# Optimization experiments

Hardware: AMD Instinct MI355X
Metric: run time of the kernel (lower is better)

## Reference

```python
import jax, jax.numpy as jnp
import numpy as np

VERY_NEG = -1e30
N_HEADS = 8


def _dag_attention(leaves, ancestors, mask, w1, b1, w2, b2):
    # leaves/ancestors: [C, A, H], mask: [C, A]
    m = mask[..., None]                                   # [C, A, 1]
    x = jnp.concatenate([leaves * m, ancestors * m], -1)  # [C, A, 2H]
    x = jax.nn.relu(x @ w1 + b1)                          # [C, A, H]
    s = x @ w2 + b2 + (1.0 - m) * VERY_NEG                # [C, A, 1]
    a = jax.nn.softmax(s, axis=1)
    return (a * ancestors * m).sum(axis=1)                # [C, H]


def _encoder_layer(x, mask4d, wq, wk, wv, wo, fw1, fb1, fw2, fb2):
    B, S, H = x.shape
    d = H // N_HEADS
    q = (x @ wq).reshape(B, S, N_HEADS, d)
    k = (x @ wk).reshape(B, S, N_HEADS, d)
    v = (x @ wv).reshape(B, S, N_HEADS, d)
    scores = jnp.einsum('bqhd,bkhd->bhqk', q, k) / jnp.sqrt(jnp.float32(d)) + mask4d
    attn = jax.nn.softmax(scores, axis=-1)
    ctx = jnp.einsum('bhqk,bkhd->bqhd', attn, v).reshape(B, S, H)
    x = x + ctx @ wo
    x = x + jax.nn.relu(x @ fw1 + fb1) @ fw2 + fb2
    return x


def _attention_pooling(x, mask3d, pw, pb):
    # x: [B, S, H], mask3d: [B, S, 1] additive mask
    s = x @ pw + pb + mask3d           # [B, S, 1]
    a = jax.nn.softmax(s, axis=1)
    return (a * x).sum(axis=1)          # [B, H]


def setup_inputs() -> dict:
    key = jax.random.key(0)
    ks = jax.random.split(key, 32)
    B, S, H, C, NODES, A = 128, 256, 256, 20000, 25000, 8

    def w(k, shape, scale=0.02):
        return (jax.random.normal(k, shape, jnp.float32) * scale)

    input_ids = jax.random.randint(ks[0], (B, S), 0, C)
    code_mask = (jax.random.uniform(ks[1], (B, S)) < 0.9).astype(jnp.float32)
    code_mask = code_mask.at[:, 0].set(1.0)
    dx_leaves_list = jax.random.randint(ks[2], (C, A), 0, NODES)
    dx_ancestors_list = jax.random.randint(ks[3], (C, A), 0, NODES)
    dx_masks_list = (jax.random.uniform(ks[4], (C, A)) < 0.8).astype(jnp.float32)
    dx_masks_list = dx_masks_list.at[:, 0].set(1.0)

    inp = dict(
        input_ids=input_ids, code_mask=code_mask,
        dx_leaves_list=dx_leaves_list, dx_ancestors_list=dx_ancestors_list,
        dx_masks_list=dx_masks_list,
        embed_init_w=w(ks[5], (NODES + 1, H)).at[NODES].set(0.0),  # padding row
        embed_inputs_w=w(ks[6], (C + 1, H)).at[C].set(0.0),
        attn_w1=w(ks[7], (2 * H, H)), attn_b1=jnp.zeros((H,), jnp.float32),
        attn_w2=w(ks[8], (H, 1)), attn_b2=jnp.zeros((1,), jnp.float32),
        pool_w=w(ks[9], (H, 1)), pool_b=jnp.zeros((1,), jnp.float32),
    )
    names = ['visit', 'dag']
    for i, nm in enumerate(names):
        base = 10 + 6 * i
        inp[nm + '_wq'] = w(ks[base], (H, H))
        inp[nm + '_wk'] = w(ks[base + 1], (H, H))
        inp[nm + '_wv'] = w(ks[base + 2], (H, H))
        inp[nm + '_wo'] = w(ks[base + 3], (H, H))
        inp[nm + '_fw1'] = w(ks[base + 4], (H, 4 * H))
        inp[nm + '_fb1'] = jnp.zeros((4 * H,), jnp.float32)
        inp[nm + '_fw2'] = w(ks[base + 5], (4 * H, H))
        inp[nm + '_fb2'] = jnp.zeros((H,), jnp.float32)
    return inp


def reference(input_ids, code_mask, dx_leaves_list, dx_ancestors_list, dx_masks_list,
              embed_init_w, embed_inputs_w, attn_w1, attn_b1, attn_w2, attn_b2,
              pool_w, pool_b,
              visit_wq, visit_wk, visit_wv, visit_wo, visit_fw1, visit_fb1, visit_fw2, visit_fb2,
              dag_wq, dag_wk, dag_wv, dag_wo, dag_fw1, dag_fb1, dag_fw2, dag_fb2):
    H = embed_init_w.shape[1]
    # Full-vocabulary DAG embedding recomputation (gather -> MLP -> masked softmax -> weighted sum)
    leaves_emb = embed_init_w[dx_leaves_list]          # [C, A, H]
    ancestors_emb = embed_init_w[dx_ancestors_list]    # [C, A, H]
    dag_emb = _dag_attention(leaves_emb, ancestors_emb, dx_masks_list,
                             attn_w1, attn_b1, attn_w2, attn_b2)   # [C, H]
    dict_matrix = jnp.concatenate([jnp.zeros((1, H), jnp.float32), dag_emb], axis=0)

    inputs = embed_inputs_w[input_ids]       # [B, S, H]
    inputs_dag = dict_matrix[input_ids]      # [B, S, H]

    ext_mask = (1.0 - code_mask)[:, None, None, :] * VERY_NEG  # [B,1,1,S]
    visit_outs = _encoder_layer(inputs, ext_mask, visit_wq, visit_wk, visit_wv, visit_wo,
                                visit_fw1, visit_fb1, visit_fw2, visit_fb2)
    dag_hidden = _encoder_layer(inputs_dag, ext_mask, dag_wq, dag_wk, dag_wv, dag_wo,
                                dag_fw1, dag_fb1, dag_fw2, dag_fb2)

    pool_mask = (1.0 - code_mask)[:, :, None] * VERY_NEG       # [B,S,1]
    dag_outs = _attention_pooling(dag_hidden, pool_mask, pool_w, pool_b)
    return (visit_outs, dag_outs)
```

## Files before the change

kernel.cpp:

```cpp
#include <hip/hip_runtime.h>
#include <hip/hip_bf16.h>
#include <math.h>

#define VERY_NEG (-1e30f)

constexpr int Bc = 128, Sc = 256, Hc = 256, Cc = 20000, Ac = 8, NHc = 8, DHc = 32, FFc = 1024;
constexpr int Mc = Bc * Sc;
constexpr int Rc = Cc * Ac;

typedef __attribute__((ext_vector_type(8))) short short8;
typedef __attribute__((ext_vector_type(4))) float floatx4;

static __device__ __forceinline__ unsigned short f2bf(float f) {
  union { float f; unsigned u; } v; v.f = f;
  unsigned r = v.u + 0x7FFF + ((v.u >> 16) & 1);
  return (unsigned short)(r >> 16);
}
static __device__ __forceinline__ unsigned pack2(float lo, float hi) {
  return (unsigned)f2bf(lo) | ((unsigned)f2bf(hi) << 16);
}
static __device__ __forceinline__ float bf2f(unsigned short u) {
  union { unsigned u; float f; } v; v.u = ((unsigned)u) << 16; return v.f;
}

static __device__ __forceinline__ void glds16(const unsigned short* g,
                                              unsigned short* l) {
  __builtin_amdgcn_global_load_lds(
      (const __attribute__((address_space(1))) void*)g,
      (__attribute__((address_space(3))) void*)l, 16, 0, 0);
}

__global__ __launch_bounds__(256) void prep_weights(
    const float* __restrict__ wq, const float* __restrict__ wk,
    const float* __restrict__ wv, const float* __restrict__ wo,
    const float* __restrict__ fw1, const float* __restrict__ fw2,
    unsigned short* __restrict__ qkvT, unsigned short* __restrict__ woT,
    unsigned short* __restrict__ fw1T, unsigned short* __restrict__ fw2T) {
  int gid = blockIdx.x * 256 + threadIdx.x;
  if (gid < 196608) {
    int which = gid >> 16, rem = gid & 65535;
    int n = rem >> 8, k = rem & 255;
    const float* w = which == 0 ? wq : (which == 1 ? wk : wv);
    qkvT[gid] = f2bf(w[k * 256 + n]);
  } else if (gid < 262144) {
    int rem = gid - 196608;
    int n = rem >> 8, k = rem & 255;
    woT[rem] = f2bf(wo[k * 256 + n]);
  } else if (gid < 524288) {
    int rem = gid - 262144;
    int n = rem >> 8, k = rem & 255;
    fw1T[rem] = f2bf(fw1[k * 1024 + n]);
  } else {
    int rem = gid - 524288;
    int n = rem >> 10, k = rem & 1023;
    fw2T[rem] = f2bf(fw2[k * 256 + n]);
  }
}

template <int K, bool BIAS, bool RELU, bool RESID, int OUT>
__global__ __launch_bounds__(256) void gemm_mfma(
    const unsigned short* __restrict__ A, const unsigned short* __restrict__ Bt,
    const float* __restrict__ bias, const float* __restrict__ resid,
    float* __restrict__ Cf, unsigned short* __restrict__ C2, int N) {
  __shared__ unsigned short As[128 * 64];
  __shared__ unsigned short Bs[128 * 64];
  const int tid = threadIdx.x;
  const int nwg = gridDim.x * gridDim.y;
  const int bid0 = blockIdx.y * gridDim.x + blockIdx.x;
  const int swz = (bid0 & 7) * (nwg >> 3) + (bid0 >> 3);
  const int rowBase = (swz / gridDim.x) * 128;
  const int colBase = (swz % gridDim.x) * 128;
  const int wave = tid >> 6, lane = tid & 63;
  const int wm = wave >> 1, wn = wave & 1;
  const int quad = lane >> 4, l15 = lane & 15;
  const int s8 = (((lane & 7) ^ (lane >> 3)) << 3);
  const int rs0 = (wave << 5) + (lane >> 3);
  const int swzf = l15 & 7;

  floatx4 acc[4][4];
#pragma unroll
  for (int mt = 0; mt < 4; ++mt)
#pragma unroll
    for (int nt = 0; nt < 4; ++nt) acc[mt][nt] = (floatx4){0.f, 0.f, 0.f, 0.f};

  for (int k0 = 0; k0 < K; k0 += 64) {
#pragma unroll
    for (int i = 0; i < 4; ++i) {
      int r = rs0 + (i << 3);
      int lb = wave * 2048 + i * 512;
      glds16(A + (size_t)(rowBase + r) * K + k0 + s8, &As[lb]);
      glds16(Bt + (size_t)(colBase + r) * K + k0 + s8, &Bs[lb]);
    }
    __syncthreads();
#pragma unroll
    for (int kk = 0; kk < 2; ++kk) {
      short8 af[4], bfr[4];
#pragma unroll
      for (int mt = 0; mt < 4; ++mt)
        af[mt] = *(const short8*)&As[(wm * 64 + mt * 16 + l15) * 64 +
                                     ((((kk << 2) | quad) ^ swzf) << 3)];
#pragma unroll
      for (int nt = 0; nt < 4; ++nt)
        bfr[nt] = *(const short8*)&Bs[(wn * 64 + nt * 16 + l15) * 64 +
                                      ((((kk << 2) | quad) ^ swzf) << 3)];
#pragma unroll
      for (int mt = 0; mt < 4; ++mt)
#pragma unroll
        for (int nt = 0; nt < 4; ++nt)
          acc[mt][nt] = __builtin_amdgcn_mfma_f32_16x16x32_bf16(
              af[mt], bfr[nt], acc[mt][nt], 0, 0, 0);
    }
    __syncthreads();
  }

#pragma unroll
  for (int mt = 0; mt < 4; ++mt) {
#pragma unroll
    for (int nt = 0; nt < 4; ++nt) {
      int col = colBase + wn * 64 + nt * 16 + l15;
      float bz = BIAS ? bias[col] : 0.f;
#pragma unroll
      for (int i = 0; i < 4; ++i) {
        int row = rowBase + wm * 64 + mt * 16 + quad * 4 + i;
        float v = acc[mt][nt][i];
        if (BIAS) v += bz;
        if (RELU) v = fmaxf(v, 0.f);
        if (RESID) v += resid[(size_t)row * N + col];
        if (OUT == 0) {
          Cf[(size_t)row * N + col] = v;
        } else if (OUT == 1) {
          C2[(size_t)row * N + col] = f2bf(v);
        } else if (OUT == 2) {
          Cf[(size_t)row * N + col] = v;
          C2[(size_t)row * N + col] = f2bf(v);
        } else {
          C2[(size_t)(col >> 8) * 16777216 + (size_t)row * 256 + (col & 255)] =
              f2bf(v);
        }
      }
    }
  }
}

__global__ __launch_bounds__(256, 2) void ffn_fused(
    const unsigned short* __restrict__ A, const unsigned short* __restrict__ w1T,
    const unsigned short* __restrict__ w2T, const float* __restrict__ b1,
    const float* __restrict__ b2, const float* __restrict__ resid,
    float* __restrict__ outC) {
  __shared__ unsigned short Xs[4][4096];
  __shared__ unsigned short Ws[16384];
  __shared__ unsigned short Hs[2][4096];
  const int tid = threadIdx.x;
  const int wave = tid >> 6, lane = tid & 63;
  const int wm = wave >> 1, wn = wave & 1;
  const int quad = lane >> 4, l15 = lane & 15;
  const int s8 = (((lane & 7) ^ (lane >> 3)) << 3);
  const int rs0x = (wave << 4) + (lane >> 3);
  const int rs0 = (wave << 5) + (lane >> 3);
  const int rs0b = (wave << 6) + (lane >> 3);
  const int swzf = l15 & 7;
  const int rowBase = blockIdx.x * 64;

#pragma unroll
  for (int kc = 0; kc < 4; ++kc)
#pragma unroll
    for (int i = 0; i < 2; ++i) {
      int r = rs0x + (i << 3);
      glds16(A + (size_t)(rowBase + r) * 256 + kc * 64 + s8,
             &Xs[kc][wave * 1024 + i * 512]);
    }

  floatx4 acc2[2][8];
#pragma unroll
  for (int mt = 0; mt < 2; ++mt)
#pragma unroll
    for (int nt = 0; nt < 8; ++nt) acc2[mt][nt] = (floatx4){0.f, 0.f, 0.f, 0.f};

  for (int nb = 0; nb < 8; ++nb) {
    floatx4 hacc[2][4];
#pragma unroll
    for (int mt = 0; mt < 2; ++mt)
#pragma unroll
      for (int nt = 0; nt < 4; ++nt) hacc[mt][nt] = (floatx4){0.f, 0.f, 0.f, 0.f};

#pragma unroll
    for (int hf = 0; hf < 2; ++hf) {
#pragma unroll
      for (int kc = 0; kc < 2; ++kc)
#pragma unroll
        for (int i = 0; i < 4; ++i) {
          int r = rs0 + (i << 3);
          glds16(w1T + (size_t)(nb * 128 + r) * 256 + (hf * 2 + kc) * 64 + s8,
                 &Ws[kc * 8192 + wave * 2048 + i * 512]);
        }
      __syncthreads();
#pragma unroll
      for (int kc = 0; kc < 2; ++kc) {
        int kg = hf * 2 + kc;
#pragma unroll
        for (int kk = 0; kk < 2; ++kk) {
          short8 af[2], bfr[4];
#pragma unroll
          for (int mt = 0; mt < 2; ++mt)
            af[mt] = *(const short8*)&Xs[kg][(wm * 32 + mt * 16 + l15) * 64 +
                                            ((((kk << 2) | quad) ^ swzf) << 3)];
#pragma unroll
          for (int nt = 0; nt < 4; ++nt)
            bfr[nt] = *(const short8*)&Ws[kc * 8192 +
                                          (wn * 64 + nt * 16 + l15) * 64 +
                                          ((((kk << 2) | quad) ^ swzf) << 3)];
#pragma unroll
          for (int mt = 0; mt < 2; ++mt)
#pragma unroll
            for (int nt = 0; nt < 4; ++nt)
              hacc[mt][nt] = __builtin_amdgcn_mfma_f32_16x16x32_bf16(
                  af[mt], bfr[nt], hacc[mt][nt], 0, 0, 0);
        }
      }
      __syncthreads();
    }

    float b1v[4];
#pragma unroll
    for (int nt = 0; nt < 4; ++nt)
      b1v[nt] = b1[nb * 128 + wn * 64 + nt * 16 + l15];
#pragma unroll
    for (int mt = 0; mt < 2; ++mt)
#pragma unroll
      for (int nt = 0; nt < 4; ++nt) {
        int nh = wn * 64 + nt * 16 + l15;
        int kc2 = nh >> 6, c6 = nh & 63;
#pragma unroll
        for (int i = 0; i < 4; ++i) {
          int row = wm * 32 + mt * 16 + quad * 4 + i;
          float hv = fmaxf(hacc[mt][nt][i] + b1v[nt], 0.f);
          Hs[kc2][row * 64 + ((((c6 >> 3) ^ (row & 7)) << 3) | (c6 & 7))] =
              f2bf(hv);
        }
      }
#pragma unroll
    for (int i = 0; i < 8; ++i) {
      int r = rs0b + (i << 3);
      glds16(w2T + (size_t)r * 1024 + nb * 128 + s8,
             &Ws[wave * 4096 + i * 512]);
    }
    __syncthreads();

#pragma unroll
    for (int kc2 = 0; kc2 < 2; ++kc2) {
      if (kc2 == 1) {
        __syncthreads();
#pragma unroll
        for (int i = 0; i < 8; ++i) {
          int r = rs0b + (i << 3);
          glds16(w2T + (size_t)r * 1024 + nb * 128 + 64 + s8,
                 &Ws[wave * 4096 + i * 512]);
        }
        __syncthreads();
      }
#pragma unroll
      for (int kk = 0; kk < 2; ++kk) {
        short8 pf[2], bfr2[8];
#pragma unroll
        for (int mt = 0; mt < 2; ++mt)
          pf[mt] = *(const short8*)&Hs[kc2][(wm * 32 + mt * 16 + l15) * 64 +
                                            ((((kk << 2) | quad) ^ swzf) << 3)];
#pragma unroll
        for (int nt = 0; nt < 8; ++nt)
          bfr2[nt] = *(const short8*)&Ws[(wn * 128 + nt * 16 + l15) * 64 +
                                         ((((kk << 2) | quad) ^ swzf) << 3)];
#pragma unroll
        for (int mt = 0; mt < 2; ++mt)
#pragma unroll
          for (int nt = 0; nt < 8; ++nt)
            acc2[mt][nt] = __builtin_amdgcn_mfma_f32_16x16x32_bf16(
                pf[mt], bfr2[nt], acc2[mt][nt], 0, 0, 0);
      }
    }
    __syncthreads();
  }

#pragma unroll
  for (int mt = 0; mt < 2; ++mt)
#pragma unroll
    for (int nt = 0; nt < 8; ++nt) {
      int col = wn * 128 + nt * 16 + l15;
      float bz = b2[col];
#pragma unroll
      for (int i = 0; i < 4; ++i) {
        int row = rowBase + wm * 32 + mt * 16 + quad * 4 + i;
        outC[(size_t)row * 256 + col] =
            acc2[mt][nt][i] + bz + resid[(size_t)row * 256 + col];
      }
    }
}

__global__ __launch_bounds__(256) void cvt_emb16(
    const float* __restrict__ emb, unsigned short* __restrict__ e16) {
  int gid = blockIdx.x * 256 + threadIdx.x;
  int base = gid * 8;
  int row = base >> 8;
  uint4 o;
  if (row < 25001) {
    float4 a = *(const float4*)(emb + base);
    float4 b = *(const float4*)(emb + base + 4);
    o.x = pack2(a.x, a.y); o.y = pack2(a.z, a.w);
    o.z = pack2(b.x, b.y); o.w = pack2(b.z, b.w);
  } else {
    o = (uint4){0u, 0u, 0u, 0u};
  }
  *(uint4*)(e16 + base) = o;
}

__global__ __launch_bounds__(256) void prep_w1T_pq(
    const float* __restrict__ w1, unsigned short* __restrict__ Bt) {
  int gid = blockIdx.x * 256 + threadIdx.x;
  int n = gid >> 8, k = gid & 255;
  float v = (n < 256) ? w1[k * 256 + n] : w1[(256 + k) * 256 + (n - 256)];
  Bt[gid] = f2bf(v);
}

__global__ __launch_bounds__(256) void dag_score(
    const int* __restrict__ leaves, const int* __restrict__ anc,
    const unsigned short* __restrict__ PQ, const float* __restrict__ b1,
    const float* __restrict__ w2, float* __restrict__ s) {
  const int tid = threadIdx.x;
  const int l16 = tid & 15;
  const int r = blockIdx.x * 16 + (tid >> 4);

  float b1c[16], w2c[16];
#pragma unroll
  for (int j = 0; j < 4; ++j) {
    *(float4*)&b1c[j * 4] = *(const float4*)(b1 + l16 * 16 + j * 4);
    *(float4*)&w2c[j * 4] = *(const float4*)(w2 + l16 * 16 + j * 4);
  }

  const int nl = leaves[r], na = anc[r];
  const unsigned short* pp = PQ + (size_t)nl * 512 + l16 * 16;
  const unsigned short* qp = PQ + (size_t)na * 512 + 256 + l16 * 16;

  float acc = 0.f;
#pragma unroll
  for (int half = 0; half < 2; ++half) {
    uint4 pv = *(const uint4*)(pp + half * 8);
    uint4 qv = *(const uint4*)(qp + half * 8);
    const unsigned short* pu = (const unsigned short*)&pv;
    const unsigned short* qu = (const unsigned short*)&qv;
#pragma unroll
    for (int j = 0; j < 8; ++j) {
      float h = bf2f(pu[j]) + bf2f(qu[j]) + b1c[half * 8 + j];
      acc += fmaxf(h, 0.f) * w2c[half * 8 + j];
    }
  }
  acc += __shfl_xor(acc, 1, 64);
  acc += __shfl_xor(acc, 2, 64);
  acc += __shfl_xor(acc, 4, 64);
  acc += __shfl_xor(acc, 8, 64);
  if (l16 == 0) s[r] = acc;
}

__global__ __launch_bounds__(256) void dag_finalize(
    const float* __restrict__ s, const float* __restrict__ masks,
    const int* __restrict__ anc, const float* __restrict__ b2,
    const unsigned short* __restrict__ emb16, float* __restrict__ dict) {
  const int c = blockIdx.x;
  const int t = threadIdx.x;
  __shared__ float sv[8], mv[8];
  __shared__ int nv[8];
  if (t < 8) {
    int idx = c * 8 + t;
    float m = masks[idx];
    sv[t] = s[idx] + b2[0] + (1.f - m) * VERY_NEG;
    mv[t] = m;
    nv[t] = anc[idx];
  }
  __syncthreads();
  float mx = -INFINITY;
#pragma unroll
  for (int a = 0; a < 8; ++a) mx = fmaxf(mx, sv[a]);
  float e[8], sum = 0.f;
#pragma unroll
  for (int a = 0; a < 8; ++a) { e[a] = __expf(sv[a] - mx); sum += e[a]; }
  float inv = 1.f / sum;
  float o = 0.f;
#pragma unroll
  for (int a = 0; a < 8; ++a)
    o += e[a] * inv * mv[a] * bf2f(emb16[(size_t)nv[a] * 256 + t]);
  dict[(size_t)(c + 1) * 256 + t] = o;
  if (c == 0) dict[t] = 0.f;
}

__global__ __launch_bounds__(256) void gather_both(
    const int* __restrict__ ids, const float4* __restrict__ table,
    float4* __restrict__ outf, unsigned short* __restrict__ outb) {
  int gid = blockIdx.x * 256 + threadIdx.x;
  int row = gid >> 6;
  int c4 = gid & 63;
  float4 v = table[(size_t)ids[row] * 64 + c4];
  outf[gid] = v;
  uint2 o;
  o.x = pack2(v.x, v.y);
  o.y = pack2(v.z, v.w);
  *(uint2*)(outb + (size_t)gid * 4) = o;
}

static __device__ __forceinline__ int vt_addr(int d, int col) {
  return d * 272 + ((((col) * 2) ^ (((d >> 3) & 3) << 4)) >> 1);
}
static __device__ __forceinline__ int ps_addr(int row, int col) {
  return row * 40 + ((((col) * 2) ^ (((row >> 2) & 3) << 4)) >> 1);
}

__global__ __launch_bounds__(256, 4) void attn_mfma(
    const unsigned short* __restrict__ q, const unsigned short* __restrict__ k,
    const unsigned short* __restrict__ v, const float* __restrict__ cm,
    unsigned short* __restrict__ ctx) {
  __shared__ unsigned short Vt[32 * 272];
  __shared__ unsigned short Ps[4][64 * 40];
  __shared__ float madd[256];
  const int b = blockIdx.x >> 3, h = blockIdx.x & 7;
  const int tid = threadIdx.x;
  const int wave = tid >> 6, lane = tid & 63;
  const int quad = lane >> 4, l15 = lane & 15;
  const size_t tokbase = (size_t)b * 256;
  const int hoff = h * 32;

#pragma unroll
  for (int it = 0; it < 4; ++it) {
    int idx = tid + it * 256;
    int row = idx >> 2, c = idx & 3;
    uint4 w = *(const uint4*)(v + (tokbase + row) * 256 + hoff + c * 8);
    const unsigned short* wsp = (const unsigned short*)&w;
#pragma unroll
    for (int j = 0; j < 8; ++j) Vt[vt_addr(c * 8 + j, row)] = wsp[j];
  }
  madd[tid] = (1.f - cm[b * 256 + tid]) * VERY_NEG;
  __syncthreads();

  short8 qf[4];
#pragma unroll
  for (int mt = 0; mt < 4; ++mt) {
    size_t qrow = tokbase + wave * 64 + mt * 16 + l15;
    qf[mt] = *(const short8*)(q + qrow * 256 + hoff + quad * 8);
  }
  float madd_r[16];
#pragma unroll
  for (int nt = 0; nt < 16; ++nt) madd_r[nt] = madd[nt * 16 + l15];

  short8 vone;
#pragma unroll
  for (int j = 0; j < 8; ++j)
    ((unsigned short*)&vone)[j] = (l15 == 0) ? 0x3F80 : 0;

  floatx4 oa[4][2], oa_l[4];
#pragma unroll
  for (int mt = 0; mt < 4; ++mt) {
    oa_l[mt] = (floatx4){0.f, 0.f, 0.f, 0.f};
#pragma unroll
    for (int nd = 0; nd < 2; ++nd) oa[mt][nd] = (floatx4){0.f, 0.f, 0.f, 0.f};
  }

  const float scale = 0.17677669529663687f;
  unsigned short* Pw = &Ps[wave][0];

  for (int t = 0; t < 4; ++t) {
    short8 kf[4];
#pragma unroll
    for (int nt = 0; nt < 4; ++nt)
      kf[nt] = *(const short8*)(k + (tokbase + t * 64 + nt * 16 + l15) * 256 +
                                hoff + quad * 8);
    floatx4 sa[4][4];
#pragma unroll
    for (int mt = 0; mt < 4; ++mt)
#pragma unroll
      for (int nt = 0; nt < 4; ++nt) sa[mt][nt] = (floatx4){0.f, 0.f, 0.f, 0.f};
#pragma unroll
    for (int mt = 0; mt < 4; ++mt)
#pragma unroll
      for (int nt = 0; nt < 4; ++nt)
        sa[mt][nt] = __builtin_amdgcn_mfma_f32_16x16x32_bf16(
            qf[mt], kf[nt], sa[mt][nt], 0, 0, 0);

#pragma unroll
    for (int ks = 0; ks < 2; ++ks) {
#pragma unroll
      for (int mt = 0; mt < 4; ++mt)
#pragma unroll
        for (int n2 = 0; n2 < 2; ++n2) {
          int nt = ks * 2 + n2;
#pragma unroll
          for (int i = 0; i < 4; ++i) {
            float p = __expf(sa[mt][nt][i] * scale + madd_r[t * 4 + nt]);
            Pw[ps_addr(mt * 16 + quad * 4 + i, n2 * 16 + l15)] = f2bf(p);
          }
        }
      __asm__ __volatile__("s_waitcnt lgkmcnt(0)" ::: "memory");
      short8 vf[2];
#pragma unroll
      for (int nd = 0; nd < 2; ++nd)
        vf[nd] = *(const short8*)&Vt[vt_addr(nd * 16 + l15,
                                             t * 64 + ks * 32 + quad * 8)];
#pragma unroll
      for (int mt = 0; mt < 4; ++mt) {
        short8 pf = *(const short8*)&Pw[ps_addr(mt * 16 + l15, quad * 8)];
#pragma unroll
        for (int nd = 0; nd < 2; ++nd)
          oa[mt][nd] = __builtin_amdgcn_mfma_f32_16x16x32_bf16(
              pf, vf[nd], oa[mt][nd], 0, 0, 0);
        oa_l[mt] = __builtin_amdgcn_mfma_f32_16x16x32_bf16(
            pf, vone, oa_l[mt], 0, 0, 0);
      }
    }
  }

  float inv[4][4];
#pragma unroll
  for (int mt = 0; mt < 4; ++mt)
#pragma unroll
    for (int i = 0; i < 4; ++i) {
      float l = __shfl(oa_l[mt][i], lane & 48, 64);
      inv[mt][i] = 1.f / l;
    }
#pragma unroll
  for (int mt = 0; mt < 4; ++mt)
#pragma unroll
    for (int nd = 0; nd < 2; ++nd)
#pragma unroll
      for (int i = 0; i < 4; ++i)
        Pw[ps_addr(mt * 16 + quad * 4 + i, nd * 16 + l15)] =
            f2bf(oa[mt][nd][i] * inv[mt][i]);
  __asm__ __volatile__("s_waitcnt lgkmcnt(0)" ::: "memory");
#pragma unroll
  for (int it = 0; it < 4; ++it) {
    int idx = it * 64 + lane;
    int row = idx >> 2, c = idx & 3;
    uint4 w = *(const uint4*)&Pw[ps_addr(row, c * 8)];
    *(uint4*)(ctx + (tokbase + wave * 64 + row) * 256 + hoff + c * 8) = w;
  }
}

__global__ __launch_bounds__(512) void pool_kernel(
    const float* __restrict__ x, const float* __restrict__ code_mask,
    const float* __restrict__ pw, const float* __restrict__ pb,
    float* __restrict__ out) {
  const int b = blockIdx.x;
  const int t = threadIdx.x;
  const int col = t & 255, half = t >> 8;
  __shared__ float ss[256];
  __shared__ float red[256];
  __shared__ float als[256];
  __shared__ float osum[512];
  const float* xb = x + (size_t)b * 256 * 256;

  if (t < 256) {
    float s = pb[0];
    for (int j = 0; j < 256; j += 4) {
      float4 xv = *(const float4*)(xb + (size_t)t * 256 + j);
      float4 wv = *(const float4*)(pw + j);
      s += xv.x * wv.x + xv.y * wv.y + xv.z * wv.z + xv.w * wv.w;
    }
    s += (1.f - code_mask[b * 256 + t]) * VERY_NEG;
    ss[t] = s; red[t] = s;
  }
  __syncthreads();
  for (int off = 128; off > 0; off >>= 1) {
    if (t < off) red[t] = fmaxf(red[t], red[t + off]);
    __syncthreads();
  }
  float m = red[0];
  __syncthreads();
  if (t < 256) {
    float e = __expf(ss[t] - m);
    als[t] = e; red[t] = e;
  }
  __syncthreads();
  for (int off = 128; off > 0; off >>= 1) {
    if (t < off) red[t] += red[t + off];
    __syncthreads();
  }
  float inv = 1.f / red[0];
  float o = 0.f;
  for (int si = half * 128; si < half * 128 + 128; ++si)
    o += als[si] * xb[(size_t)si * 256 + col];
  osum[t] = o;
  __syncthreads();
  if (t < 256) out[b * 256 + t] = (osum[t] + osum[t + 256]) * inv;
}

extern "C" void kernel_launch(void* const* d_in, const int* in_sizes, int n_in,
                              void* d_out, int out_size, void* d_ws,
                              size_t ws_size, hipStream_t stream) {
  const int* input_ids = (const int*)d_in[0];
  const float* code_mask = (const float*)d_in[1];
  const int* dx_leaves = (const int*)d_in[2];
  const int* dx_anc = (const int*)d_in[3];
  const float* dx_masks = (const float*)d_in[4];
  const float* embed_init_w = (const float*)d_in[5];
  const float* embed_inputs_w = (const float*)d_in[6];
  const float* attn_w1 = (const float*)d_in[7];
  const float* attn_b1 = (const float*)d_in[8];
  const float* attn_w2 = (const float*)d_in[9];
  const float* attn_b2 = (const float*)d_in[10];
  const float* pool_w = (const float*)d_in[11];
  const float* pool_b = (const float*)d_in[12];

  float* out = (float*)d_out;
  float* ws = (float*)d_ws;

  float* dict = ws;
  float* xbuf = dict + 5120256;
  float* qb   = xbuf + 8388608;
  float* kb   = qb + 8388608;
  float* vb   = kb + 8388608;
  float* ctxb = vb + 8388608;
  float* wend = ctxb + 8388608;

  unsigned short* emb16  = (unsigned short*)xbuf;
  unsigned short* pq16   = (unsigned short*)(xbuf + 3211264);
  unsigned short* w1T_pq = (unsigned short*)kb;
  float* sbuf = vb;

  unsigned short* xb16  = (unsigned short*)ctxb;
  unsigned short* qkv16 = (unsigned short*)qb;
  unsigned short* xq16  = (unsigned short*)qb;
  unsigned short* qkvT = (unsigned short*)wend;
  unsigned short* woT  = qkvT + 196608;
  unsigned short* fw1T = woT + 65536;
  unsigned short* fw2T = fw1T + 262144;

  cvt_emb16<<<3136, 256, 0, stream>>>(embed_init_w, emb16);
  prep_w1T_pq<<<512, 256, 0, stream>>>(attn_w1, w1T_pq);
  gemm_mfma<256, false, false, false, 1><<<dim3(4, 196), 256, 0, stream>>>(
      emb16, w1T_pq, nullptr, nullptr, nullptr, pq16, 512);
  dag_score<<<Rc / 16, 256, 0, stream>>>(dx_leaves, dx_anc, pq16, attn_b1,
                                         attn_w2, sbuf);
  dag_finalize<<<Cc, 256, 0, stream>>>(sbuf, dx_masks, dx_anc, attn_b2,
                                       emb16, dict);

  auto run_encoder = [&](const float* wq, const float* wk, const float* wv,
                         const float* wo, const float* fw1, const float* fb1,
                         const float* fw2, const float* fb2, float* final_out) {
    prep_weights<<<3072, 256, 0, stream>>>(wq, wk, wv, wo, fw1, fw2, qkvT,
                                           woT, fw1T, fw2T);
    gemm_mfma<256, false, false, false, 3><<<dim3(6, 256), 256, 0, stream>>>(
        xb16, qkvT, nullptr, nullptr, nullptr, qkv16, 256);
    attn_mfma<<<Bc * NHc, 256, 0, stream>>>(qkv16, qkv16 + 16777216,
                                            qkv16 + 33554432, code_mask, xb16);
    gemm_mfma<256, false, false, true, 2><<<dim3(2, 256), 256, 0, stream>>>(
        xb16, woT, nullptr, xbuf, xbuf, xq16, 256);
    ffn_fused<<<512, 256, 0, stream>>>(xq16, fw1T, fw2T, fb1, fb2, xbuf,
                                       final_out);
  };

  gather_both<<<8192, 256, 0, stream>>>(input_ids,
                                        (const float4*)embed_inputs_w,
                                        (float4*)xbuf, xb16);
  run_encoder((const float*)d_in[13], (const float*)d_in[14],
              (const float*)d_in[15], (const float*)d_in[16],
              (const float*)d_in[17], (const float*)d_in[18],
              (const float*)d_in[19], (const float*)d_in[20], out);

  gather_both<<<8192, 256, 0, stream>>>(input_ids, (const float4*)dict,
                                        (float4*)xbuf, xb16);
  run_encoder((const float*)d_in[21], (const float*)d_in[22],
              (const float*)d_in[23], (const float*)d_in[24],
              (const float*)d_in[25], (const float*)d_in[26],
              (const float*)d_in[27], (const float*)d_in[28], xbuf);

  pool_kernel<<<Bc, 512, 0, stream>>>(xbuf, code_mask, pool_w, pool_b,
                                      out + 8388608);
}
```

Measured before the change: 563.2 us.

## Restructure fused FFN to 128-row tiles with register-resident activations; tile weight transpose

The fused FFN kernel now runs 512 threads per block over 128 rows instead of 64. Input activation fragments are loaded once into registers, and each step stages the full K=256 slab of w1 and a 256x128 w2 slab in shared memory, which cuts barriers and per-step reloads. The weight prep kernel becomes a 64x64 shared-memory tiled transpose with vectorized loads and stores, replacing strided scalar reads. The trade-off is a larger shared-memory footprint (about 96KB) and higher register pressure per block, which likely limits the kernel to one block per CU.

```diff
diff --git a/kernel.cpp b/kernel.cpp
--- a/kernel.cpp
+++ b/kernel.cpp
@@ -36,25 +36,40 @@
     const float* __restrict__ fw1, const float* __restrict__ fw2,
     unsigned short* __restrict__ qkvT, unsigned short* __restrict__ woT,
     unsigned short* __restrict__ fw1T, unsigned short* __restrict__ fw2T) {
-  int gid = blockIdx.x * 256 + threadIdx.x;
-  if (gid < 196608) {
-    int which = gid >> 16, rem = gid & 65535;
-    int n = rem >> 8, k = rem & 255;
-    const float* w = which == 0 ? wq : (which == 1 ? wk : wv);
-    qkvT[gid] = f2bf(w[k * 256 + n]);
-  } else if (gid < 262144) {
-    int rem = gid - 196608;
-    int n = rem >> 8, k = rem & 255;
-    woT[rem] = f2bf(wo[k * 256 + n]);
-  } else if (gid < 524288) {
-    int rem = gid - 262144;
-    int n = rem >> 8, k = rem & 255;
-    fw1T[rem] = f2bf(fw1[k * 1024 + n]);
+  __shared__ float T[64][65];
+  const int t = blockIdx.x;
+  const float* src;
+  unsigned short* dst;
+  int R, Cn, tr, tc;
+  if (t < 64) {
+    int m = t >> 4, tt = t & 15;
+    src = m == 0 ? wq : (m == 1 ? wk : (m == 2 ? wv : wo));
+    dst = m < 3 ? qkvT + m * 65536 : woT;
+    R = 256; Cn = 256; tr = tt >> 2; tc = tt & 3;
+  } else if (t < 128) {
+    int tt = t - 64;
+    src = fw1; dst = fw1T; R = 256; Cn = 1024;
+    tr = tt >> 4; tc = tt & 15;
   } else {
-    int rem = gid - 524288;
-    int n = rem >> 10, k = rem & 1023;
-    fw2T[rem] = f2bf(fw2[k * 256 + n]);
-  }
+    int tt = t - 128;
+    src = fw2; dst = fw2T; R = 1024; Cn = 256;
+    tr = tt >> 2; tc = tt & 3;
+  }
+  const int r0 = threadIdx.x >> 4, c4 = threadIdx.x & 15;
+#pragma unroll
+  for (int it = 0; it < 4; ++it) {
+    int row = it * 16 + r0;
+    *(float4*)&T[row][c4 * 4] =
+        *(const float4*)(src + (size_t)(tr * 64 + row) * Cn + tc * 64 + c4 * 4);
+  }
+  __syncthreads();
+  const int c0 = threadIdx.x >> 2, seg = threadIdx.x & 3;
+  unsigned short tmp[16];
+#pragma unroll
+  for (int j = 0; j < 16; ++j) tmp[j] = f2bf(T[seg * 16 + j][c0]);
+  unsigned short* dp = dst + (size_t)(tc * 64 + c0) * R + tr * 64 + seg * 16;
+  *(uint4*)dp = *(uint4*)&tmp[0];
+  *(uint4*)(dp + 8) = *(uint4*)&tmp[8];
 }
 
 template <int K, bool BIAS, bool RELU, bool RESID, int OUT>
@@ -142,33 +157,41 @@
   }
 }
 
-__global__ __launch_bounds__(256, 2) void ffn_fused(
+__global__ __launch_bounds__(512, 2) void ffn_fused(
     const unsigned short* __restrict__ A, const unsigned short* __restrict__ w1T,
     const unsigned short* __restrict__ w2T, const float* __restrict__ b1,
     const float* __restrict__ b2, const float* __restrict__ resid,
     float* __restrict__ outC) {
-  __shared__ unsigned short Xs[4][4096];
-  __shared__ unsigned short Ws[16384];
-  __shared__ unsigned short Hs[2][4096];
+  __shared__ unsigned short WsA[32768];
+  __shared__ unsigned short Hs[16384];
   const int tid = threadIdx.x;
   const int wave = tid >> 6, lane = tid & 63;
   const int wm = wave >> 1, wn = wave & 1;
   const int quad = lane >> 4, l15 = lane & 15;
   const int s8 = (((lane & 7) ^ (lane >> 3)) << 3);
-  const int rs0x = (wave << 4) + (lane >> 3);
-  const int rs0 = (wave << 5) + (lane >> 3);
-  const int rs0b = (wave << 6) + (lane >> 3);
-  const int swzf = l15 & 7;
-  const int rowBase = blockIdx.x * 64;
+  const int swz = l15 & 7;
+  const int rowBase = blockIdx.x * 128;
 
 #pragma unroll
   for (int kc = 0; kc < 4; ++kc)
 #pragma unroll
     for (int i = 0; i < 2; ++i) {
-      int r = rs0x + (i << 3);
-      glds16(A + (size_t)(rowBase + r) * 256 + kc * 64 + s8,
-             &Xs[kc][wave * 1024 + i * 512]);
-    }
+      int rb = wave * 16 + i * 8;
+      glds16(A + (size_t)(rowBase + rb + (lane >> 3)) * 256 + kc * 64 + s8,
+             &WsA[kc * 8192 + rb * 64]);
+    }
+  __syncthreads();
+  short8 af[2][8];
+#pragma unroll
+  for (int mt = 0; mt < 2; ++mt) {
+    int row = wm * 32 + mt * 16 + l15;
+#pragma unroll
+    for (int gk = 0; gk < 8; ++gk)
+      af[mt][gk] =
+          *(const short8*)&WsA[(gk >> 1) * 8192 + row * 64 +
+                               (((((gk & 1) << 2) | quad) ^ swz) << 3)];
+  }
+  __syncthreads();
 
   floatx4 acc2[2][8];
 #pragma unroll
@@ -177,47 +200,36 @@
     for (int nt = 0; nt < 8; ++nt) acc2[mt][nt] = (floatx4){0.f, 0.f, 0.f, 0.f};
 
   for (int nb = 0; nb < 8; ++nb) {
+#pragma unroll
+    for (int kc = 0; kc < 4; ++kc)
+#pragma unroll
+      for (int i = 0; i < 2; ++i) {
+        int rb = wave * 16 + i * 8;
+        glds16(w1T + (size_t)(nb * 128 + rb + (lane >> 3)) * 256 + kc * 64 + s8,
+               &WsA[kc * 8192 + rb * 64]);
+      }
+    __syncthreads();
+
     floatx4 hacc[2][4];
 #pragma unroll
     for (int mt = 0; mt < 2; ++mt)
 #pragma unroll
       for (int nt = 0; nt < 4; ++nt) hacc[mt][nt] = (floatx4){0.f, 0.f, 0.f, 0.f};
-
-#pragma unroll
-    for (int hf = 0; hf < 2; ++hf) {
-#pragma unroll
-      for (int kc = 0; kc < 2; ++kc)
-#pragma unroll
-        for (int i = 0; i < 4; ++i) {
-          int r = rs0 + (i << 3);
-          glds16(w1T + (size_t)(nb * 128 + r) * 256 + (hf * 2 + kc) * 64 + s8,
-                 &Ws[kc * 8192 + wave * 2048 + i * 512]);
-        }
-      __syncthreads();
-#pragma unroll
-      for (int kc = 0; kc < 2; ++kc) {
-        int kg = hf * 2 + kc;
-#pragma unroll
-        for (int kk = 0; kk < 2; ++kk) {
-          short8 af[2], bfr[4];
-#pragma unroll
-          for (int mt = 0; mt < 2; ++mt)
-            af[mt] = *(const short8*)&Xs[kg][(wm * 32 + mt * 16 + l15) * 64 +
-                                            ((((kk << 2) | quad) ^ swzf) << 3)];
-#pragma unroll
-          for (int nt = 0; nt < 4; ++nt)
-            bfr[nt] = *(const short8*)&Ws[kc * 8192 +
-                                          (wn * 64 + nt * 16 + l15) * 64 +
-                                          ((((kk << 2) | quad) ^ swzf) << 3)];
-#pragma unroll
-          for (int mt = 0; mt < 2; ++mt)
-#pragma unroll
-            for (int nt = 0; nt < 4; ++nt)
-              hacc[mt][nt] = __builtin_amdgcn_mfma_f32_16x16x32_bf16(
-                  af[mt], bfr[nt], hacc[mt][nt], 0, 0, 0);
-        }
-      }
-      __syncthreads();
+#pragma unroll
+    for (int gk = 0; gk < 8; ++gk) {
+      short8 bfr[4];
+#pragma unroll
+      for (int nt = 0; nt < 4; ++nt) {
+        int rw = wn * 64 + nt * 16 + l15;
+        bfr[nt] = *(const short8*)&WsA[(gk >> 1) * 8192 + rw * 64 +
+                                       (((((gk & 1) << 2) | quad) ^ swz) << 3)];
+      }
+#pragma unroll
+      for (int mt = 0; mt < 2; ++mt)
+#pragma unroll
+        for (int nt = 0; nt < 4; ++nt)
+          hacc[mt][nt] = __builtin_amdgcn_mfma_f32_16x16x32_bf16(
+              af[mt][gk], bfr[nt], hacc[mt][nt], 0, 0, 0);
     }
 
     float b1v[4];
@@ -228,54 +240,49 @@
     for (int mt = 0; mt < 2; ++mt)
 #pragma unroll
       for (int nt = 0; nt < 4; ++nt) {
-        int nh = wn * 64 + nt * 16 + l15;
-        int kc2 = nh >> 6, c6 = nh & 63;
+        int c = wn * 64 + nt * 16 + l15;
+        int hc = c >> 6, c6 = c & 63;
 #pragma unroll
         for (int i = 0; i < 4; ++i) {
           int row = wm * 32 + mt * 16 + quad * 4 + i;
           float hv = fmaxf(hacc[mt][nt][i] + b1v[nt], 0.f);
-          Hs[kc2][row * 64 + ((((c6 >> 3) ^ (row & 7)) << 3) | (c6 & 7))] =
-              f2bf(hv);
+          Hs[hc * 8192 + row * 64 +
+             ((((c6 >> 3) ^ (row & 7)) << 3) | (c6 & 7))] = f2bf(hv);
         }
       }
-#pragma unroll
-    for (int i = 0; i < 8; ++i) {
-      int r = rs0b + (i << 3);
-      glds16(w2T + (size_t)r * 1024 + nb * 128 + s8,
-             &Ws[wave * 4096 + i * 512]);
-    }
-    __syncthreads();
-
-#pragma unroll
-    for (int kc2 = 0; kc2 < 2; ++kc2) {
-      if (kc2 == 1) {
-        __syncthreads();
-#pragma unroll
-        for (int i = 0; i < 8; ++i) {
-          int r = rs0b + (i << 3);
-          glds16(w2T + (size_t)r * 1024 + nb * 128 + 64 + s8,
-                 &Ws[wave * 4096 + i * 512]);
-        }
-        __syncthreads();
-      }
-#pragma unroll
-      for (int kk = 0; kk < 2; ++kk) {
-        short8 pf[2], bfr2[8];
-#pragma unroll
-        for (int mt = 0; mt < 2; ++mt)
-          pf[mt] = *(const short8*)&Hs[kc2][(wm * 32 + mt * 16 + l15) * 64 +
-                                            ((((kk << 2) | quad) ^ swzf) << 3)];
+    __syncthreads();
+
+#pragma unroll
+    for (int kc = 0; kc < 2; ++kc)
+#pragma unroll
+      for (int i = 0; i < 4; ++i) {
+        int rb = wave * 32 + i * 8;
+        glds16(w2T + (size_t)(rb + (lane >> 3)) * 1024 + nb * 128 + kc * 64 + s8,
+               &WsA[kc * 16384 + rb * 64]);
+      }
+    __syncthreads();
+
+#pragma unroll
+    for (int gk = 0; gk < 4; ++gk) {
+      short8 pf[2], bfr2[8];
+#pragma unroll
+      for (int mt = 0; mt < 2; ++mt) {
+        int row = wm * 32 + mt * 16 + l15;
+        pf[mt] = *(const short8*)&Hs[(gk >> 1) * 8192 + row * 64 +
+                                     (((((gk & 1) << 2) | quad) ^ swz) << 3)];
+      }
+#pragma unroll
+      for (int nt = 0; nt < 8; ++nt) {
+        int rw = wn * 128 + nt * 16 + l15;
+        bfr2[nt] = *(const short8*)&WsA[(gk >> 1) * 16384 + rw * 64 +
+                                        (((((gk & 1) << 2) | quad) ^ swz) << 3)];
+      }
+#pragma unroll
+      for (int mt = 0; mt < 2; ++mt)
 #pragma unroll
         for (int nt = 0; nt < 8; ++nt)
-          bfr2[nt] = *(const short8*)&Ws[(wn * 128 + nt * 16 + l15) * 64 +
-                                         ((((kk << 2) | quad) ^ swzf) << 3)];
-#pragma unroll
-        for (int mt = 0; mt < 2; ++mt)
-#pragma unroll
-          for (int nt = 0; nt < 8; ++nt)
-            acc2[mt][nt] = __builtin_amdgcn_mfma_f32_16x16x32_bf16(
-                pf[mt], bfr2[nt], acc2[mt][nt], 0, 0, 0);
-      }
+          acc2[mt][nt] = __builtin_amdgcn_mfma_f32_16x16x32_bf16(
+              pf[mt], bfr2[nt], acc2[mt][nt], 0, 0, 0);
     }
     __syncthreads();
   }
@@ -640,15 +647,15 @@
   auto run_encoder = [&](const float* wq, const float* wk, const float* wv,
                          const float* wo, const float* fw1, const float* fb1,
                          const float* fw2, const float* fb2, float* final_out) {
-    prep_weights<<<3072, 256, 0, stream>>>(wq, wk, wv, wo, fw1, fw2, qkvT,
-                                           woT, fw1T, fw2T);
+    prep_weights<<<192, 256, 0, stream>>>(wq, wk, wv, wo, fw1, fw2, qkvT,
+                                          woT, fw1T, fw2T);
     gemm_mfma<256, false, false, false, 3><<<dim3(6, 256), 256, 0, stream>>>(
         xb16, qkvT, nullptr, nullptr, nullptr, qkv16, 256);
     attn_mfma<<<Bc * NHc, 256, 0, stream>>>(qkv16, qkv16 + 16777216,
                                             qkv16 + 33554432, code_mask, xb16);
     gemm_mfma<256, false, false, true, 2><<<dim3(2, 256), 256, 0, stream>>>(
         xb16, woT, nullptr, xbuf, xbuf, xq16, 256);
-    ffn_fused<<<512, 256, 0, stream>>>(xq16, fw1T, fw2T, fb1, fb2, xbuf,
+    ffn_fused<<<256, 512, 0, stream>>>(xq16, fw1T, fw2T, fb1, fb2, xbuf,
                                        final_out);
   };
 
```

Result: no change. 556.2 us (-1.3%).
